# Performance work log

Measured on AMD Instinct MI355X. Metric: run time of the kernel, lower is better.

The kernel has to match this reference:

```python
import jax, jax.numpy as jnp
import numpy as np

AT = 4000

def _make_alphas(lower=0.01, upper=3.0, at=AT):
    # generate_alphas: alpha_t = (1-(t-1)/AT)*lower + ((t-1)/AT)*upper, t=1..AT (t=1 gives lower)
    t = jnp.arange(1, at + 1, dtype=jnp.float32)
    a = (1.0 - (t - 1.0) / at) * lower + ((t - 1.0) / at) * upper
    return a[:, None]  # [AT, 1]

def setup_inputs() -> dict:
    key = jax.random.key(0)
    kx, kg, kw, ki = jax.random.split(key, 4)
    b, N, p = 128, 100, 12
    x = jax.random.normal(kx, (b, N, p), dtype=jnp.float32)
    g = jax.random.uniform(kg, (N * N, N * N), dtype=jnp.float32)          # fixed graph kernel, non-trainable
    weights = jax.random.uniform(kw, (N * N, 1), dtype=jnp.float32)        # nn.init.uniform_ default U(0,1)
    alphas = _make_alphas()                                                # deterministic buffer [AT,1]
    x_i = jax.random.randint(ki, (b, p), 0, AT)                            # steps into the AT axis
    return {"x": x, "g": g, "weights": weights, "alphas": alphas, "x_i": x_i}

def reference(x, g, weights, alphas, x_i):
    # x: [b,N,p], g: [N*N,N*N], weights: [N*N,1], alphas: [AT,1], x_i: [b,p] int
    N = x.shape[1]
    F = g @ (weights ** 2)                         # [N*N, 1]
    W = alphas @ (-F.T)                            # [AT, N*N]
    f = jax.nn.softmax(W.reshape(-1, N, N), -1)    # [AT, N, N] row-softmax transition matrices
    # Fused version of the per-feature loop: one gather + single einsum accumulate.
    fg = f[x_i]                                    # [b, p, N, N]
    Z = jnp.einsum('bpnm,bmp->bn', fg, x)          # sum_p f[x_i[:,p]] @ x[:,:,p]
    return Z, F
```

## Files before the change

kernel.cpp:

```cpp
#include <hip/hip_runtime.h>

#define NROW 10000
#define NN   100
#define PP   12
#define BB   128
#define RPB  8

typedef float f32x4 __attribute__((ext_vector_type(4)));

__global__ void w2_kernel(const float* __restrict__ w, float* __restrict__ w2) {
    int i = blockIdx.x * 256 + threadIdx.x;
    if (i < NROW) { float v = w[i]; w2[i] = v * v; }
}

__global__ __launch_bounds__(512) void f_kernel(const float* __restrict__ g,
                                                const float* __restrict__ w2,
                                                float* __restrict__ Fout) {
    const int tid  = threadIdx.x;
    const int wave = tid >> 6;
    const int lane = tid & 63;
    const int row  = blockIdx.x * RPB + wave;

    const f32x4* grow = (const f32x4*)(g + (size_t)row * NROW);
    const f32x4* wv4  = (const f32x4*)w2;
    f32x4 acc4 = {0.f, 0.f, 0.f, 0.f};
    #pragma unroll 4
    for (int c = lane; c < NROW / 4; c += 64) {
        acc4 += __builtin_nontemporal_load(&grow[c]) * wv4[c];
    }
    float acc = acc4.x + acc4.y + acc4.z + acc4.w;
    #pragma unroll
    for (int off = 32; off > 0; off >>= 1) acc += __shfl_down(acc, off, 64);
    if (lane == 0) Fout[row] = acc;
}

__global__ __launch_bounds__(512) void z_kernel(const float* __restrict__ x,
                                                const float* __restrict__ alphas,
                                                const int*   __restrict__ xi,
                                                const float* __restrict__ F,
                                                float* __restrict__ Z) {
    const int b = blockIdx.x;
    __shared__ float Fs[NN * 101];
    __shared__ float xs[NN * PP];
    __shared__ float al[PP];
    const int tid = threadIdx.x;

    for (int j = tid; j < NROW; j += 512)
        Fs[(j / NN) * 101 + (j % NN)] = F[j];
    for (int j = tid; j < NN * PP; j += 512)
        xs[j] = x[(size_t)b * (NN * PP) + j];
    if (tid < PP) al[tid] = alphas[xi[b * PP + tid]];
    __syncthreads();

    const int n = tid >> 2;
    const int q = tid & 3;
    if (n < NN) {
        const float* Fr = &Fs[n * 101];

        float rmin = Fr[q * 25];
        #pragma unroll
        for (int m = 1; m < 25; m++) rmin = fminf(rmin, Fr[q * 25 + m]);
        rmin = fminf(rmin, __shfl_xor(rmin, 1, 64));
        rmin = fminf(rmin, __shfl_xor(rmin, 2, 64));

        float zacc = 0.f;
        #pragma unroll
        for (int pp = 0; pp < 3; pp++) {
            const int p = q * 3 + pp;
            const float a = al[p];
            float num = 0.f, den = 0.f;
            for (int m = 0; m < NN; m++) {
                float e = __expf(a * (rmin - Fr[m]));
                num += e * xs[m * PP + p];
                den += e;
            }
            zacc += num / den;
        }
        zacc += __shfl_xor(zacc, 1, 64);
        zacc += __shfl_xor(zacc, 2, 64);
        if (q == 0) Z[b * NN + n] = zacc;
    }
}

extern "C" void kernel_launch(void* const* d_in, const int* in_sizes, int n_in,
                              void* d_out, int out_size, void* d_ws, size_t ws_size,
                              hipStream_t stream) {
    const float* x      = (const float*)d_in[0];
    const float* g      = (const float*)d_in[1];
    const float* w      = (const float*)d_in[2];
    const float* alphas = (const float*)d_in[3];
    const int*   xi     = (const int*)d_in[4];

    float* Z  = (float*)d_out;
    float* F  = (float*)d_out + BB * NN;
    float* w2 = (float*)d_ws;

    w2_kernel<<<(NROW + 255) / 256, 256, 0, stream>>>(w, w2);
    f_kernel<<<NROW / RPB, 512, 0, stream>>>(g, w2, F);
    z_kernel<<<BB, 512, 0, stream>>>(x, alphas, xi, F, Z);
}
```

Baseline: 89.61 us.

## Split z_kernel across row quarters and unroll f_kernel GEMV deeper

```diff
diff --git a/kernel.cpp b/kernel.cpp
--- a/kernel.cpp
+++ b/kernel.cpp
@@ -17,20 +17,23 @@
                                                 const float* __restrict__ w2,
                                                 float* __restrict__ Fout) {
     const int tid  = threadIdx.x;
-    const int wave = tid >> 6;
     const int lane = tid & 63;
-    const int row  = blockIdx.x * RPB + wave;
+    const int row  = blockIdx.x * RPB + (tid >> 6);
 
     const f32x4* grow = (const f32x4*)(g + (size_t)row * NROW);
     const f32x4* wv4  = (const f32x4*)w2;
     f32x4 acc4 = {0.f, 0.f, 0.f, 0.f};
-    #pragma unroll 4
-    for (int c = lane; c < NROW / 4; c += 64) {
-        acc4 += __builtin_nontemporal_load(&grow[c]) * wv4[c];
-    }
+
+    int c = lane;
+    #pragma unroll 8
+    for (; c < 2496; c += 64)
+        acc4 += __builtin_nontemporal_load(grow + c) * wv4[c];
+    if (c < NROW / 4)
+        acc4 += __builtin_nontemporal_load(grow + c) * wv4[c];
+
     float acc = acc4.x + acc4.y + acc4.z + acc4.w;
     #pragma unroll
-    for (int off = 32; off > 0; off >>= 1) acc += __shfl_down(acc, off, 64);
+    for (int off = 32; off; off >>= 1) acc += __shfl_down(acc, off, 64);
     if (lane == 0) Fout[row] = acc;
 }
 
@@ -39,46 +42,52 @@
                                                 const int*   __restrict__ xi,
                                                 const float* __restrict__ F,
                                                 float* __restrict__ Z) {
-    const int b = blockIdx.x;
-    __shared__ float Fs[NN * 101];
+    const int bid = blockIdx.x;
+    const int b   = bid >> 2;
+    const int nq  = bid & 3;
+    const int n0  = nq * 25;
+    __shared__ float Fs[25 * 101];
     __shared__ float xs[NN * PP];
     __shared__ float al[PP];
     const int tid = threadIdx.x;
 
-    for (int j = tid; j < NROW; j += 512)
-        Fs[(j / NN) * 101 + (j % NN)] = F[j];
+    for (int j = tid; j < 25 * NN; j += 512) {
+        int r = j / NN, m = j - r * NN;
+        Fs[r * 101 + m] = F[(n0 + r) * NN + m];
+    }
     for (int j = tid; j < NN * PP; j += 512)
         xs[j] = x[(size_t)b * (NN * PP) + j];
     if (tid < PP) al[tid] = alphas[xi[b * PP + tid]];
     __syncthreads();
 
-    const int n = tid >> 2;
-    const int q = tid & 3;
-    if (n < NN) {
-        const float* Fr = &Fs[n * 101];
+    const int nl = tid >> 4;
+    const int q  = tid & 15;
+    if (nl < 25) {
+        const float* Fr = &Fs[nl * 101];
 
-        float rmin = Fr[q * 25];
-        #pragma unroll
-        for (int m = 1; m < 25; m++) rmin = fminf(rmin, Fr[q * 25 + m]);
+        float rmin = 3.4e38f;
+        for (int m = q; m < NN; m += 16) rmin = fminf(rmin, Fr[m]);
         rmin = fminf(rmin, __shfl_xor(rmin, 1, 64));
         rmin = fminf(rmin, __shfl_xor(rmin, 2, 64));
+        rmin = fminf(rmin, __shfl_xor(rmin, 4, 64));
+        rmin = fminf(rmin, __shfl_xor(rmin, 8, 64));
 
         float zacc = 0.f;
-        #pragma unroll
-        for (int pp = 0; pp < 3; pp++) {
-            const int p = q * 3 + pp;
-            const float a = al[p];
+        if (q < PP) {
+            const float a = al[q];
             float num = 0.f, den = 0.f;
             for (int m = 0; m < NN; m++) {
                 float e = __expf(a * (rmin - Fr[m]));
-                num += e * xs[m * PP + p];
+                num += e * xs[m * PP + q];
                 den += e;
             }
-            zacc += num / den;
+            zacc = num / den;
         }
         zacc += __shfl_xor(zacc, 1, 64);
         zacc += __shfl_xor(zacc, 2, 64);
-        if (q == 0) Z[b * NN + n] = zacc;
+        zacc += __shfl_xor(zacc, 4, 64);
+        zacc += __shfl_xor(zacc, 8, 64);
+        if (q == 0) Z[b * NN + n0 + nl] = zacc;
     }
 }
 
@@ -97,5 +106,5 @@
 
     w2_kernel<<<(NROW + 255) / 256, 256, 0, stream>>>(w, w2);
     f_kernel<<<NROW / RPB, 512, 0, stream>>>(g, w2, F);
-    z_kernel<<<BB, 512, 0, stream>>>(x, alphas, xi, F, Z);
+    z_kernel<<<BB * 4, 512, 0, stream>>>(x, alphas, xi, F, Z);
 }
```

Result: faster. 82.26 us (-8.2%).
